# Kernel tuning notes

Hardware: AMD Instinct MI355X
Metric: run time of the kernel (lower is better)

## Reference

```python
import jax, jax.numpy as jnp
import numpy as np

H = 12          # num_heads
E = 768         # key_dim
LORA_SCALE = 32.0 / 4.0  # scale / R
NEG = -1e9


def setup_inputs() -> dict:
    key = jax.random.key(0)
    ks = jax.random.split(key, 8)
    B, L = 2, 2048
    return {
        "x": jax.random.normal(ks[0], (B, L, E), jnp.float32),
        "w_in": jax.random.normal(ks[1], (E, 3 * E), jnp.float32) * 0.02,
        "b_in": jnp.zeros((3 * E,), jnp.float32),
        "A_in": jax.random.normal(ks[2], (4, 3 * E), jnp.float32) * 0.02,
        "B_in": jax.random.normal(ks[3], (E, 4), jnp.float32) * 0.02,
        "w_out": jax.random.normal(ks[4], (E, E), jnp.float32) * 0.02,
        "b_out": jnp.zeros((E,), jnp.float32),
        "A_out": jax.random.normal(ks[5], (4, E), jnp.float32) * 0.02,
        "B_out": jax.random.normal(ks[6], (E, 4), jnp.float32) * 0.02,
    }


def reference(x, w_in, b_in, A_in, B_in, w_out, b_out, A_out, B_out):
    Bb, L, _ = x.shape
    D = E // H
    # LoRA-adapted input projection: w + (scale/R) * B @ A
    w1 = w_in + LORA_SCALE * (B_in @ A_in)          # [E, 3E]
    c = jnp.einsum('ble,eo->blo', x, w1) + b_in      # [B, L, 3E]
    q, k, v = jnp.split(c, 3, axis=2)
    # split heads -> [B, H, L, D]
    def heads(t):
        return t.reshape(Bb, L, H, D).transpose(0, 2, 1, 3)
    q, k, v = heads(q), heads(k), heads(v)
    # attention scores (no 1/sqrt(d): scale=False in module defaults)
    w = jnp.einsum('bhqd,bhkd->bhqk', q, k)          # [B, H, L, L]
    band = jnp.tril(jnp.ones((L, L), jnp.float32))   # causal band
    w = w * band + NEG * (1.0 - band)
    w = jax.nn.softmax(w, axis=-1)
    a = jnp.einsum('bhqk,bhkd->bhqd', w, v)          # [B, H, L, D]
    a = a.transpose(0, 2, 1, 3).reshape(Bb, L, E)    # merge heads
    w2 = w_out + LORA_SCALE * (B_out @ A_out)        # [E, E]
    return jnp.einsum('ble,eo->blo', a, w2) + b_out
```

## Files before the change

### kernel.cpp

```cpp
#include <hip/hip_runtime.h>
#include <hip/hip_bf16.h>

#define BB 2
#define LL 2048
#define EE 768
#define HH 12
#define DD 64
#define N3 2304
#define TOK 4096
#define LOG2E 1.4426950408889634f

typedef __attribute__((ext_vector_type(8))) short short8;
typedef __attribute__((ext_vector_type(4))) short s16x4;
typedef __attribute__((ext_vector_type(4))) float f32x4;
typedef __attribute__((ext_vector_type(4))) unsigned int uix4;
typedef unsigned int uint_t;
typedef unsigned short ushort_t;

__device__ __forceinline__ f32x4 mfma16(short8 a, short8 b, f32x4 c) {
  return __builtin_amdgcn_mfma_f32_16x16x32_bf16(a, b, c, 0, 0, 0);
}
__device__ __forceinline__ f32x4 mfma16k16(s16x4 a, s16x4 b, f32x4 c) {
  return __builtin_amdgcn_mfma_f32_16x16x16bf16_1k(a, b, c, 0, 0, 0);
}

__device__ __forceinline__ ushort_t bf16bits(float f) {
  __hip_bfloat16 h = __float2bfloat16(f);
  return *reinterpret_cast<ushort_t*>(&h);
}

__device__ __forceinline__ float fast_exp2(float x) {
  float r;
  asm("v_exp_f32 %0, %1" : "=v"(r) : "v"(x));
  return r;
}

__device__ __forceinline__ uint_t pack2bf_rn(float a, float b) {
  uint_t ua = __float_as_uint(a) + 0x8000u;
  uint_t ub = __float_as_uint(b) + 0x8000u;
  return (ua >> 16) | (ub & 0xFFFF0000u);
}

__device__ __forceinline__ float bits2f(ushort_t u) {
  union { uint_t u; float f; } cv;
  cv.u = ((uint_t)u) << 16;
  return cv.f;
}

__device__ __forceinline__ void stage64(const __hip_bfloat16* gbase, int ldg,
                                        short* lds, int tid) {
  const int wave = tid >> 6, lane = tid & 63;
#pragma unroll
  for (int c = 0; c < 4; ++c) {
    int off = c * 4096 + wave * 1024 + lane * 16;
    int row = off >> 7;
    int cs  = (off & 127) >> 4;
    int cc  = cs ^ (row & 7);
    __builtin_amdgcn_global_load_lds(
        (const __attribute__((address_space(1))) void*)((const short*)gbase + (size_t)row * ldg + cc * 8),
        (__attribute__((address_space(3))) void*)(lds + c * 2048 + wave * 512),
        16, 0, 0);
  }
}

__device__ __forceinline__ void stage64h(const __hip_bfloat16* gbase, int ldg,
                                         short* lds, int tid) {
  const int wave = tid >> 6, lane = tid & 63;
#pragma unroll
  for (int c = 0; c < 2; ++c) {
    int off = c * 4096 + wave * 1024 + lane * 16;
    int row = off >> 7;
    int cs  = (off & 127) >> 4;
    int cc  = cs ^ (row & 7);
    __builtin_amdgcn_global_load_lds(
        (const __attribute__((address_space(1))) void*)((const short*)gbase + (size_t)row * ldg + cc * 8),
        (__attribute__((address_space(3))) void*)(lds + c * 2048 + wave * 512),
        16, 0, 0);
  }
}

__device__ __forceinline__ short8 frag64(const short* lds, int row, int chunk) {
  return *(const short8*)(lds + row * 64 + (chunk ^ (row & 7)) * 8);
}

__global__ void prep_kernel(const float* __restrict__ x, const float* __restrict__ w_in,
                            const float* __restrict__ A_in, const float* __restrict__ B_in,
                            const float* __restrict__ w_out, const float* __restrict__ A_out,
                            const float* __restrict__ B_out,
                            __hip_bfloat16* __restrict__ xb, __hip_bfloat16* __restrict__ w1T,
                            __hip_bfloat16* __restrict__ w2T) {
  __shared__ float tile[32][33];
  const int bid = blockIdx.x, t = threadIdx.x;
  if (bid < 2304) {
    const float *W, *Am, *Bm;
    __hip_bfloat16* out;
    int N, tx, ty;
    if (bid < 1728) { W = w_in;  Am = A_in;  Bm = B_in;  out = w1T; N = N3; tx = bid % 72; ty = bid / 72; }
    else { int jj = bid - 1728; W = w_out; Am = A_out; Bm = B_out; out = w2T; N = EE; tx = jj % 24; ty = jj / 24; }
    const int e0 = ty * 32, o0 = tx * 32;
    const int r = t >> 5, col = t & 31;
#pragma unroll
    for (int i = 0; i < 4; ++i)
      tile[r + i * 8][col] = W[(size_t)(e0 + r + i * 8) * N + (o0 + col)];
    __syncthreads();
    const int e = e0 + col;
    const float b0 = Bm[e * 4 + 0], b1 = Bm[e * 4 + 1], b2 = Bm[e * 4 + 2], b3 = Bm[e * 4 + 3];
#pragma unroll
    for (int i = 0; i < 4; ++i) {
      const int o = o0 + r + i * 8;
      float acc = b0 * Am[o] + b1 * Am[N + o] + b2 * Am[2 * N + o] + b3 * Am[3 * N + o];
      out[(size_t)o * EE + e] = __float2bfloat16(tile[col][r + i * 8] + 8.0f * acc);
    }
  } else {
    const int j = bid - 2304;
    const float* src = x + (size_t)j * 4096 + t * 16;
    short* dst = (short*)xb + (size_t)j * 4096 + t * 16;
#pragma unroll
    for (int half = 0; half < 2; ++half) {
      float4 a = ((const float4*)src)[half * 2];
      float4 b = ((const float4*)src)[half * 2 + 1];
      short8 v;
      v[0] = (short)bf16bits(a.x); v[1] = (short)bf16bits(a.y);
      v[2] = (short)bf16bits(a.z); v[3] = (short)bf16bits(a.w);
      v[4] = (short)bf16bits(b.x); v[5] = (short)bf16bits(b.y);
      v[6] = (short)bf16bits(b.z); v[7] = (short)bf16bits(b.w);
      ((short8*)dst)[half] = v;
    }
  }
}

template<int NT, bool F32OUT, bool QSCALE, bool SPLITV>
__global__ __launch_bounds__(256, 3) void gemm_bt(const __hip_bfloat16* __restrict__ A,
                                                  const __hip_bfloat16* __restrict__ BT,
                                                  const float* __restrict__ bias,
                                                  void* __restrict__ outp,
                                                  __hip_bfloat16* __restrict__ vTp,
                                                  int M, int N, int K) {
  constexpr int NACC = NT / 32;
  __shared__ __align__(16) short Al[128 * 64];
  __shared__ __align__(16) short Bl[NT * 64];
  const int tid = threadIdx.x, lane = tid & 63, wave = tid >> 6;
  const int quad = lane >> 4, c16 = lane & 15;
  const int n0 = blockIdx.x * NT, m0 = blockIdx.y * 128;
  const int msub = (wave & 1) * 64, nsub = (wave >> 1) * (NT / 2);
  f32x4 acc[4][NACC] = {};
  for (int k0 = 0; k0 < K; k0 += 64) {
    __syncthreads();
    stage64(A + (size_t)m0 * K + k0, K, Al, tid);
    if (NT == 128) stage64(BT + (size_t)n0 * K + k0, K, Bl, tid);
    else           stage64h(BT + (size_t)n0 * K + k0, K, Bl, tid);
    __syncthreads();
#pragma unroll
    for (int ks = 0; ks < 2; ++ks) {
      short8 af[4], bfr[NACC];
#pragma unroll
      for (int i = 0; i < 4; ++i)
        af[i] = frag64(Al, msub + i * 16 + c16, ks * 4 + quad);
#pragma unroll
      for (int i = 0; i < NACC; ++i)
        bfr[i] = frag64(Bl, nsub + i * 16 + c16, ks * 4 + quad);
#pragma unroll
      for (int mi = 0; mi < 4; ++mi)
#pragma unroll
        for (int ni = 0; ni < NACC; ++ni)
          acc[mi][ni] = mfma16(af[mi], bfr[ni], acc[mi][ni]);
    }
  }
  if (SPLITV && n0 >= 2 * EE) {
    const int bofs = (m0 >> 11) * EE;
    const int l0 = (m0 & 2047) + msub;
#pragma unroll
    for (int ni = 0; ni < NACC; ++ni) {
      int n = n0 + nsub + ni * 16 + c16;
      float bv = bias[n];
      const size_t rowbase = (size_t)(bofs + (n - 2 * EE)) * LL;
#pragma unroll
      for (int mi = 0; mi < 4; ++mi) {
        int l = l0 + mi * 16 + quad * 4;
        uint2 w;
        w.x = pack2bf_rn(acc[mi][ni][0] + bv, acc[mi][ni][1] + bv);
        w.y = pack2bf_rn(acc[mi][ni][2] + bv, acc[mi][ni][3] + bv);
        *(uint2*)((short*)vTp + rowbase + l) = w;
      }
    }
    return;
  }
#pragma unroll
  for (int ni = 0; ni < NACC; ++ni) {
    int n = n0 + nsub + ni * 16 + c16;
    float bv = bias[n];
    float sc = (QSCALE && n < EE) ? LOG2E : 1.0f;
#pragma unroll
    for (int mi = 0; mi < 4; ++mi) {
      int row0 = m0 + msub + mi * 16 + quad * 4;
#pragma unroll
      for (int r = 0; r < 4; ++r) {
        float v = (acc[mi][ni][r] + bv) * sc;
        if (F32OUT) ((float*)outp)[(size_t)(row0 + r) * N + n] = v;
        else ((__hip_bfloat16*)outp)[(size_t)(row0 + r) * N + n] = __float2bfloat16(v);
      }
    }
  }
}

#define SLOT_BYTES 16896
union pk4 { uint_t u[2]; s16x4 s4; };

__device__ const signed char QTAB[40] = {
  3,4,5,6,7,8,9,10,11,12,13,14,15,  7,8,9,10,11,12,13,14,15,
  11,12,13,14,15, 15,  2,6,10,14,  1,5,9,13,  0,4,8,12};
__device__ const signed char CTAB[40] = {
  0,0,0,0,0,0,0,0,0,0,0,0,0,  1,1,1,1,1,1,1,1,1,
  2,2,2,2,2, 3,  0,1,2,3,  0,1,2,3,  0,1,2,3};

__global__ __launch_bounds__(256, 4) void attn_kernel(const __hip_bfloat16* __restrict__ qkv,
                                                      const __hip_bfloat16* __restrict__ vT,
                                                      char* __restrict__ Opart,
                                                      __hip_bfloat16* __restrict__ abuf) {
  __shared__ __align__(16) short Kl[2 * 64 * 64];
  __shared__ __align__(16) short Vl[2 * 64 * 64];
  const int tid = threadIdx.x, lane = tid & 63, wave = tid >> 6;
  const int quad = lane >> 4, c16 = lane & 15;
  const int bid = blockIdx.x;
  const int bh = bid % 24;
  const int j = bid / 24;
  const int qt = QTAB[j], cch = CTAB[j];
  const int b = bh / HH, h = bh % HH;
  const int q0 = qt * 128;
  const int qw = q0 + wave * 32;
  const int ks = cch * 512;
  const int ke = min(q0 + 128, ks + 512);
  const int niter = (ke - ks + 63) >> 6;
  short8 qfA[2], qfB[2];
  {
    const short* qra = (const short*)qkv + (size_t)(b * LL + qw + c16) * N3 + h * DD;
    qfA[0] = *(const short8*)(qra + quad * 8);
    qfA[1] = *(const short8*)(qra + 32 + quad * 8);
    const short* qrb = qra + 16 * N3;
    qfB[0] = *(const short8*)(qrb + quad * 8);
    qfB[1] = *(const short8*)(qrb + 32 + quad * 8);
  }
  float lA = 0.f, lB = 0.f;
  f32x4 oA[4] = {}, oB[4] = {};
  const int vsub = (quad & 1) * 4;
  const int cxor = (c16 & 7);
  const __hip_bfloat16* kgbase = qkv + (size_t)(b * LL) * N3 + EE + h * DD;
  const __hip_bfloat16* vgbase = vT + (size_t)((b * HH + h) * DD) * LL;
  stage64h(kgbase + (size_t)ks * N3, N3, Kl, tid);
  stage64h(vgbase + ks, LL, Vl, tid);
  for (int it = 0; it < niter; ++it) {
    const int k0 = ks + it * 64;
    __syncthreads();
    if (it + 1 < niter) {
      short* Kn = Kl + ((it + 1) & 1) * 4096;
      short* Vn = Vl + ((it + 1) & 1) * 4096;
      stage64h(kgbase + (size_t)(k0 + 64) * N3, N3, Kn, tid);
      stage64h(vgbase + k0 + 64, LL, Vn, tid);
    }
    const short* Kb = Kl + (it & 1) * 4096;
    const short* Vb = Vl + (it & 1) * 4096;
    int nlimB = (qw + 31 - k0) / 16 + 1; if (nlimB > 4) nlimB = 4;
    int nlimA = (qw + 15 - k0) / 16 + 1; if (nlimA > 4) nlimA = 4;
#pragma unroll
    for (int nt = 0; nt < 4; ++nt) {
      if (nt < nlimB) {
        const short* krow = Kb + (nt * 16 + c16) * 64;
        const int kc0 = (quad ^ cxor) * 8;
        short8 kf0 = *(const short8*)(krow + kc0);
        short8 kf1 = *(const short8*)(krow + (kc0 ^ 32));
        const int kb = k0 + nt * 16 + quad * 4;
        const bool diag = (k0 + nt * 16 + 15 > qw + 16);
        f32x4 sB = {};
        sB = mfma16(kf0, qfB[0], sB);
        sB = mfma16(kf1, qfB[1], sB);
        if (diag) {
          const int q = qw + 16 + c16;
#pragma unroll
          for (int r = 0; r < 4; ++r)
            if (kb + r > q) sB[r] = -1e9f;
        }
        pk4 pB;
        {
          float p0 = fast_exp2(sB[0]), p1 = fast_exp2(sB[1]);
          float p2 = fast_exp2(sB[2]), p3 = fast_exp2(sB[3]);
          lB += (p0 + p1) + (p2 + p3);
          pB.u[0] = pack2bf_rn(p0, p1);
          pB.u[1] = pack2bf_rn(p2, p3);
        }
        const bool doA = (nt < nlimA);
        pk4 pA;
        if (doA) {
          f32x4 sA = {};
          sA = mfma16(kf0, qfA[0], sA);
          sA = mfma16(kf1, qfA[1], sA);
          if (k0 + nt * 16 + 15 > qw) {
            const int q = qw + c16;
#pragma unroll
            for (int r = 0; r < 4; ++r)
              if (kb + r > q) sA[r] = -1e9f;
          }
          float p0 = fast_exp2(sA[0]), p1 = fast_exp2(sA[1]);
          float p2 = fast_exp2(sA[2]), p3 = fast_exp2(sA[3]);
          lA += (p0 + p1) + (p2 + p3);
          pA.u[0] = pack2bf_rn(p0, p1);
          pA.u[1] = pack2bf_rn(p2, p3);
        }
        const int cg = (nt * 2 + (quad >> 1)) ^ cxor;
        const short* vbase = Vb + c16 * 64 + cg * 8 + vsub;
#pragma unroll
        for (int dt = 0; dt < 4; ++dt) {
          s16x4 vf = *(const s16x4*)(vbase + dt * 1024);
          oB[dt] = mfma16k16(vf, pB.s4, oB[dt]);
          if (doA) oA[dt] = mfma16k16(vf, pA.s4, oA[dt]);
        }
      }
    }
  }
  lA += __shfl_xor(lA, 16); lA += __shfl_xor(lA, 32);
  lB += __shfl_xor(lB, 16); lB += __shfl_xor(lB, 32);
  const bool single = (cch == 0) && (qt < 4);
  const float nA = single ? 1.0f / lA : 1.0f;
  const float nB = single ? 1.0f / lB : 1.0f;
  char* op = Opart + (size_t)((bh * 16 + qt) * 4 + cch) * SLOT_BYTES;
  if (!single && quad == 0) {
    float* lout = (float*)(op + 16384);
    lout[wave * 32 + c16] = lA;
    lout[wave * 32 + 16 + c16] = lB;
  }
  __syncthreads();
  short* reg = Kl + wave * 1152;
#pragma unroll
  for (int hh = 0; hh < 2; ++hh) {
    const float sc = hh ? nB : nA;
#pragma unroll
    for (int dt = 0; dt < 4; ++dt) {
      f32x4 o = hh ? oB[dt] : oA[dt];
      uint_t* p = (uint_t*)(reg + c16 * 72 + dt * 16 + quad * 4);
      p[0] = pack2bf_rn(o[0] * sc, o[1] * sc);
      p[1] = pack2bf_rn(o[2] * sc, o[3] * sc);
    }
#pragma unroll
    for (int it = 0; it < 2; ++it) {
      int idx = it * 64 + lane;
      int tq = idx >> 3, c = idx & 7;
      short8 v = *(const short8*)(reg + tq * 72 + c * 8);
      if (single)
        *(short8*)((short*)abuf + (size_t)(b * LL + q0 + wave * 32 + hh * 16 + tq) * EE + h * DD + c * 8) = v;
      else
        *(short8*)((short*)op + (wave * 32 + hh * 16 + tq) * 64 + c * 8) = v;
    }
  }
}

__global__ void merge_kernel(const char* __restrict__ Opart,
                             __hip_bfloat16* __restrict__ abuf) {
  const int t = threadIdx.x;
  const int bh = blockIdx.x / 12, qt = 4 + (blockIdx.x % 12);
  const int nch = (qt >> 2) + 1;
  const int b = bh / HH, h = bh % HH;
  const char* pb = Opart + (size_t)((bh * 16 + qt) * 4) * SLOT_BYTES;
  const int q = t >> 1, dc = (t & 1) * 32;
  float l = 0.f;
  float acc[32];
#pragma unroll
  for (int i = 0; i < 32; ++i) acc[i] = 0.f;
#pragma unroll
  for (int c = 0; c < 4; ++c) {
    if (c < nch) {
      const char* p = pb + (size_t)c * SLOT_BYTES;
      l += ((const float*)(p + 16384))[q];
      const short* o = (const short*)p + q * 64 + dc;
#pragma unroll
      for (int blk = 0; blk < 4; ++blk) {
        short8 r = *(const short8*)(o + blk * 8);
#pragma unroll
        for (int i = 0; i < 8; ++i) acc[blk * 8 + i] += bits2f((ushort_t)r[i]);
      }
    }
  }
  const float inv = 1.0f / l;
  __align__(16) short out[32];
#pragma unroll
  for (int i = 0; i < 16; ++i)
    ((uint_t*)out)[i] = pack2bf_rn(acc[2 * i] * inv, acc[2 * i + 1] * inv);
  short* dst = (short*)abuf + (size_t)(b * LL + qt * 128 + q) * EE + h * DD + dc;
#pragma unroll
  for (int blk = 0; blk < 4; ++blk)
    *(short8*)(dst + blk * 8) = *(short8*)(out + blk * 8);
}

extern "C" void kernel_launch(void* const* d_in, const int* in_sizes, int n_in,
                              void* d_out, int out_size, void* d_ws, size_t ws_size,
                              hipStream_t stream) {
  (void)in_sizes; (void)n_in; (void)out_size; (void)ws_size;
  const float* x     = (const float*)d_in[0];
  const float* w_in  = (const float*)d_in[1];
  const float* b_in  = (const float*)d_in[2];
  const float* A_in  = (const float*)d_in[3];
  const float* B_in  = (const float*)d_in[4];
  const float* w_out = (const float*)d_in[5];
  const float* b_out = (const float*)d_in[6];
  const float* A_out = (const float*)d_in[7];
  const float* B_out = (const float*)d_in[8];
  char* ws = (char*)d_ws;
  __hip_bfloat16* xb   = (__hip_bfloat16*)(ws);
  __hip_bfloat16* w1T  = (__hip_bfloat16*)(ws + 6291456);
  __hip_bfloat16* w2T  = (__hip_bfloat16*)(ws + 9830400);
  __hip_bfloat16* qkv  = (__hip_bfloat16*)(ws + 11010048);
  __hip_bfloat16* vT   = (__hip_bfloat16*)(ws + 29884416);
  __hip_bfloat16* abuf = (__hip_bfloat16*)(ws + 36175872);
  char* Opart          = ws + 42467328;

  prep_kernel<<<3072, 256, 0, stream>>>(x, w_in, A_in, B_in, w_out, A_out, B_out,
                                        xb, w1T, w2T);
  gemm_bt<128, false, true, true><<<dim3(N3 / 128, TOK / 128), 256, 0, stream>>>(
      xb, w1T, b_in, qkv, vT, TOK, N3, EE);
  attn_kernel<<<24 * 40, 256, 0, stream>>>(qkv, vT, Opart, abuf);
  merge_kernel<<<24 * 12, 256, 0, stream>>>(Opart, abuf);
  gemm_bt<64, true, false, false><<<dim3(EE / 64, TOK / 128), 256, 0, stream>>>(
      abuf, w2T, b_out, d_out, nullptr, TOK, EE, EE);
}
```

Baseline: 156.1 us.

## Fuse split-KV attention merge into output projection GEMM A-tile staging

Drops the separate merge kernel. The output-projection GEMM now combines the partial attention outputs and normalisers from Opart while staging its A tile for the multi-chunk query tiles (qt>=4). Tiles with a single chunk still read abuf directly. This removes one launch and the abuf write/read round trip, but the merge work is repeated in every N-column block (12x redundancy) and uses synchronous loads instead of async global_load_lds. Attention launch bounds also rise from 4 to 5 blocks per CU.

```diff
diff --git a/kernel.cpp b/kernel.cpp
--- a/kernel.cpp
+++ b/kernel.cpp
@@ -46,6 +46,8 @@
   cv.u = ((uint_t)u) << 16;
   return cv.f;
 }
+
+#define SLOT_BYTES 16896
 
 __device__ __forceinline__ void stage64(const __hip_bfloat16* gbase, int ldg,
                                         short* lds, int tid) {
@@ -129,12 +131,13 @@
   }
 }
 
-template<int NT, bool F32OUT, bool QSCALE, bool SPLITV>
+template<int NT, bool F32OUT, bool QSCALE, bool SPLITV, bool FUSE>
 __global__ __launch_bounds__(256, 3) void gemm_bt(const __hip_bfloat16* __restrict__ A,
                                                   const __hip_bfloat16* __restrict__ BT,
                                                   const float* __restrict__ bias,
                                                   void* __restrict__ outp,
                                                   __hip_bfloat16* __restrict__ vTp,
+                                                  const char* __restrict__ OpartP,
                                                   int M, int N, int K) {
   constexpr int NACC = NT / 32;
   __shared__ __align__(16) short Al[128 * 64];
@@ -143,10 +146,43 @@
   const int quad = lane >> 4, c16 = lane & 15;
   const int n0 = blockIdx.x * NT, m0 = blockIdx.y * 128;
   const int msub = (wave & 1) * 64, nsub = (wave >> 1) * (NT / 2);
+  const int qt = (m0 & 2047) >> 7;
   f32x4 acc[4][NACC] = {};
   for (int k0 = 0; k0 < K; k0 += 64) {
     __syncthreads();
-    stage64(A + (size_t)m0 * K + k0, K, Al, tid);
+    if (FUSE && qt >= 4) {
+      const int nch = (qt >> 2) + 1;
+      const int bh = (m0 >> 11) * HH + (k0 >> 6);
+      const char* pb = OpartP + (size_t)((bh * 16 + qt) * 4) * SLOT_BYTES;
+#pragma unroll
+      for (int c = 0; c < 4; ++c) {
+        int off = c * 4096 + wave * 1024 + lane * 16;
+        int row = off >> 7;
+        int cs  = (off & 127) >> 4;
+        int cc  = cs ^ (row & 7);
+        float l = 0.f;
+        float a8[8] = {};
+#pragma unroll
+        for (int ch = 0; ch < 4; ++ch) {
+          if (ch < nch) {
+            const char* p = pb + (size_t)ch * SLOT_BYTES;
+            l += ((const float*)(p + 16384))[row];
+            short8 v = *(const short8*)((const short*)p + row * 64 + cc * 8);
+#pragma unroll
+            for (int i = 0; i < 8; ++i) a8[i] += bits2f((ushort_t)v[i]);
+          }
+        }
+        const float inv = 1.0f / l;
+        short8 w;
+        ((uint_t*)&w)[0] = pack2bf_rn(a8[0] * inv, a8[1] * inv);
+        ((uint_t*)&w)[1] = pack2bf_rn(a8[2] * inv, a8[3] * inv);
+        ((uint_t*)&w)[2] = pack2bf_rn(a8[4] * inv, a8[5] * inv);
+        ((uint_t*)&w)[3] = pack2bf_rn(a8[6] * inv, a8[7] * inv);
+        *(short8*)(Al + c * 2048 + wave * 512 + lane * 8) = w;
+      }
+    } else {
+      stage64(A + (size_t)m0 * K + k0, K, Al, tid);
+    }
     if (NT == 128) stage64(BT + (size_t)n0 * K + k0, K, Bl, tid);
     else           stage64h(BT + (size_t)n0 * K + k0, K, Bl, tid);
     __syncthreads();
@@ -203,7 +239,6 @@
   }
 }
 
-#define SLOT_BYTES 16896
 union pk4 { uint_t u[2]; s16x4 s4; };
 
 __device__ const signed char QTAB[40] = {
@@ -213,7 +248,7 @@
   0,0,0,0,0,0,0,0,0,0,0,0,0,  1,1,1,1,1,1,1,1,1,
   2,2,2,2,2, 3,  0,1,2,3,  0,1,2,3,  0,1,2,3};
 
-__global__ __launch_bounds__(256, 4) void attn_kernel(const __hip_bfloat16* __restrict__ qkv,
+__global__ __launch_bounds__(256, 5) void attn_kernel(const __hip_bfloat16* __restrict__ qkv,
                                                       const __hip_bfloat16* __restrict__ vT,
                                                       char* __restrict__ Opart,
                                                       __hip_bfloat16* __restrict__ abuf) {
@@ -352,43 +387,6 @@
   }
 }
 
-__global__ void merge_kernel(const char* __restrict__ Opart,
-                             __hip_bfloat16* __restrict__ abuf) {
-  const int t = threadIdx.x;
-  const int bh = blockIdx.x / 12, qt = 4 + (blockIdx.x % 12);
-  const int nch = (qt >> 2) + 1;
-  const int b = bh / HH, h = bh % HH;
-  const char* pb = Opart + (size_t)((bh * 16 + qt) * 4) * SLOT_BYTES;
-  const int q = t >> 1, dc = (t & 1) * 32;
-  float l = 0.f;
-  float acc[32];
-#pragma unroll
-  for (int i = 0; i < 32; ++i) acc[i] = 0.f;
-#pragma unroll
-  for (int c = 0; c < 4; ++c) {
-    if (c < nch) {
-      const char* p = pb + (size_t)c * SLOT_BYTES;
-      l += ((const float*)(p + 16384))[q];
-      const short* o = (const short*)p + q * 64 + dc;
-#pragma unroll
-      for (int blk = 0; blk < 4; ++blk) {
-        short8 r = *(const short8*)(o + blk * 8);
-#pragma unroll
-        for (int i = 0; i < 8; ++i) acc[blk * 8 + i] += bits2f((ushort_t)r[i]);
-      }
-    }
-  }
-  const float inv = 1.0f / l;
-  __align__(16) short out[32];
-#pragma unroll
-  for (int i = 0; i < 16; ++i)
-    ((uint_t*)out)[i] = pack2bf_rn(acc[2 * i] * inv, acc[2 * i + 1] * inv);
-  short* dst = (short*)abuf + (size_t)(b * LL + qt * 128 + q) * EE + h * DD + dc;
-#pragma unroll
-  for (int blk = 0; blk < 4; ++blk)
-    *(short8*)(dst + blk * 8) = *(short8*)(out + blk * 8);
-}
-
 extern "C" void kernel_launch(void* const* d_in, const int* in_sizes, int n_in,
                               void* d_out, int out_size, void* d_ws, size_t ws_size,
                               hipStream_t stream) {
@@ -413,10 +411,9 @@
 
   prep_kernel<<<3072, 256, 0, stream>>>(x, w_in, A_in, B_in, w_out, A_out, B_out,
                                         xb, w1T, w2T);
-  gemm_bt<128, false, true, true><<<dim3(N3 / 128, TOK / 128), 256, 0, stream>>>(
-      xb, w1T, b_in, qkv, vT, TOK, N3, EE);
+  gemm_bt<128, false, true, true, false><<<dim3(N3 / 128, TOK / 128), 256, 0, stream>>>(
+      xb, w1T, b_in, qkv, vT, nullptr, TOK, N3, EE);
   attn_kernel<<<24 * 40, 256, 0, stream>>>(qkv, vT, Opart, abuf);
-  merge_kernel<<<24 * 12, 256, 0, stream>>>(Opart, abuf);
-  gemm_bt<64, true, false, false><<<dim3(EE / 64, TOK / 128), 256, 0, stream>>>(
-      abuf, w2T, b_out, d_out, nullptr, TOK, EE, EE);
-}
+  gemm_bt<64, true, false, false, true><<<dim3(EE / 64, TOK / 128), 256, 0, stream>>>(
+      abuf, w2T, b_out, d_out, nullptr, Opart, TOK, EE, EE);
+}
```

Measured after the change: 205.8 us. 31.9% more time.

## Double-buffer GEMM LDS tiles with K-step 32 to overlap loads and MFMA

Applied to the files above, without the earlier changes.

Rewrites the bf16 GEMM main loop to use two LDS buffers of 32-wide K slices. The loads for the next slice are issued before the MFMAs on the current slice, leaving one barrier per iteration. New stage32/frag32 helpers use a 4-way XOR swizzle for the narrower rows. The aim is to hide global-to-LDS latency behind compute, at the cost of twice as many loop iterations and barriers for the same K.

```diff
diff --git a/kernel.cpp b/kernel.cpp
--- a/kernel.cpp
+++ b/kernel.cpp
@@ -47,20 +47,39 @@
   return cv.f;
 }
 
-__device__ __forceinline__ void stage64(const __hip_bfloat16* gbase, int ldg,
+#define SLOT_BYTES 16896
+
+__device__ __forceinline__ void stage32(const __hip_bfloat16* gbase, int ldg,
                                         short* lds, int tid) {
   const int wave = tid >> 6, lane = tid & 63;
 #pragma unroll
-  for (int c = 0; c < 4; ++c) {
+  for (int c = 0; c < 2; ++c) {
     int off = c * 4096 + wave * 1024 + lane * 16;
-    int row = off >> 7;
-    int cs  = (off & 127) >> 4;
-    int cc  = cs ^ (row & 7);
+    int row = off >> 6;
+    int cs  = (off & 63) >> 4;
+    int cc  = cs ^ (row & 3);
     __builtin_amdgcn_global_load_lds(
         (const __attribute__((address_space(1))) void*)((const short*)gbase + (size_t)row * ldg + cc * 8),
         (__attribute__((address_space(3))) void*)(lds + c * 2048 + wave * 512),
         16, 0, 0);
   }
+}
+
+__device__ __forceinline__ void stage32h(const __hip_bfloat16* gbase, int ldg,
+                                         short* lds, int tid) {
+  const int wave = tid >> 6, lane = tid & 63;
+  int off = wave * 1024 + lane * 16;
+  int row = off >> 6;
+  int cs  = (off & 63) >> 4;
+  int cc  = cs ^ (row & 3);
+  __builtin_amdgcn_global_load_lds(
+      (const __attribute__((address_space(1))) void*)((const short*)gbase + (size_t)row * ldg + cc * 8),
+      (__attribute__((address_space(3))) void*)(lds + wave * 512),
+      16, 0, 0);
+}
+
+__device__ __forceinline__ short8 frag32(const short* lds, int row, int quad) {
+  return *(const short8*)(lds + row * 32 + ((quad ^ (row & 3)) << 3));
 }
 
 __device__ __forceinline__ void stage64h(const __hip_bfloat16* gbase, int ldg,
@@ -77,10 +96,6 @@
         (__attribute__((address_space(3))) void*)(lds + c * 2048 + wave * 512),
         16, 0, 0);
   }
-}
-
-__device__ __forceinline__ short8 frag64(const short* lds, int row, int chunk) {
-  return *(const short8*)(lds + row * 64 + (chunk ^ (row & 7)) * 8);
 }
 
 __global__ void prep_kernel(const float* __restrict__ x, const float* __restrict__ w_in,
@@ -137,34 +152,42 @@
                                                   __hip_bfloat16* __restrict__ vTp,
                                                   int M, int N, int K) {
   constexpr int NACC = NT / 32;
-  __shared__ __align__(16) short Al[128 * 64];
-  __shared__ __align__(16) short Bl[NT * 64];
+  constexpr int BHALF = NT * 32;
+  __shared__ __align__(16) short Al[2 * 128 * 32];
+  __shared__ __align__(16) short Bl[2 * BHALF];
   const int tid = threadIdx.x, lane = tid & 63, wave = tid >> 6;
   const int quad = lane >> 4, c16 = lane & 15;
   const int n0 = blockIdx.x * NT, m0 = blockIdx.y * 128;
   const int msub = (wave & 1) * 64, nsub = (wave >> 1) * (NT / 2);
+  const int niter = K >> 5;
   f32x4 acc[4][NACC] = {};
-  for (int k0 = 0; k0 < K; k0 += 64) {
+  stage32(A + (size_t)m0 * K, K, Al, tid);
+  if (NT == 128) stage32(BT + (size_t)n0 * K, K, Bl, tid);
+  else           stage32h(BT + (size_t)n0 * K, K, Bl, tid);
+  for (int it = 0; it < niter; ++it) {
     __syncthreads();
-    stage64(A + (size_t)m0 * K + k0, K, Al, tid);
-    if (NT == 128) stage64(BT + (size_t)n0 * K + k0, K, Bl, tid);
-    else           stage64h(BT + (size_t)n0 * K + k0, K, Bl, tid);
-    __syncthreads();
-#pragma unroll
-    for (int ks = 0; ks < 2; ++ks) {
-      short8 af[4], bfr[NACC];
-#pragma unroll
-      for (int i = 0; i < 4; ++i)
-        af[i] = frag64(Al, msub + i * 16 + c16, ks * 4 + quad);
-#pragma unroll
-      for (int i = 0; i < NACC; ++i)
-        bfr[i] = frag64(Bl, nsub + i * 16 + c16, ks * 4 + quad);
-#pragma unroll
-      for (int mi = 0; mi < 4; ++mi)
-#pragma unroll
-        for (int ni = 0; ni < NACC; ++ni)
-          acc[mi][ni] = mfma16(af[mi], bfr[ni], acc[mi][ni]);
-    }
+    if (it + 1 < niter) {
+      const int k1 = (it + 1) << 5;
+      short* An = Al + ((it + 1) & 1) * 4096;
+      short* Bn = Bl + ((it + 1) & 1) * BHALF;
+      stage32(A + (size_t)m0 * K + k1, K, An, tid);
+      if (NT == 128) stage32(BT + (size_t)n0 * K + k1, K, Bn, tid);
+      else           stage32h(BT + (size_t)n0 * K + k1, K, Bn, tid);
+    }
+    const short* Ab = Al + (it & 1) * 4096;
+    const short* Bb = Bl + (it & 1) * BHALF;
+    short8 af[4], bfr[NACC];
+#pragma unroll
+    for (int i = 0; i < 4; ++i)
+      af[i] = frag32(Ab, msub + i * 16 + c16, quad);
+#pragma unroll
+    for (int i = 0; i < NACC; ++i)
+      bfr[i] = frag32(Bb, nsub + i * 16 + c16, quad);
+#pragma unroll
+    for (int mi = 0; mi < 4; ++mi)
+#pragma unroll
+      for (int ni = 0; ni < NACC; ++ni)
+        acc[mi][ni] = mfma16(af[mi], bfr[ni], acc[mi][ni]);
   }
   if (SPLITV && n0 >= 2 * EE) {
     const int bofs = (m0 >> 11) * EE;
@@ -203,7 +226,6 @@
   }
 }
 
-#define SLOT_BYTES 16896
 union pk4 { uint_t u[2]; s16x4 s4; };
 
 __device__ const signed char QTAB[40] = {
```

New measurement: 163.1 us. 4.5% more time.
